# Optimization experiments

Measured on AMD Instinct MI355X. Metric: run time of the kernel, lower is better.

## Reference

```python
import jax, jax.numpy as jnp
import numpy as np

B, D, T, H = 1024, 128, 256, 64  # batch, input_dim, seq_len, hidden_dim


def _lstm_layer(x_proj, w_hh):
    """x_proj: [B, T, 4H] precomputed input projection (incl. both biases).
    Returns (all hidden states [B, T, H], final hidden [B, H])."""
    b = x_proj.shape[0]
    h0 = jnp.zeros((b, H), x_proj.dtype)
    c0 = jnp.zeros((b, H), x_proj.dtype)

    def step(carry, xt):
        h, c = carry
        gates = xt + h @ w_hh.T  # [B, 4H]; PyTorch gate order i, f, g, o
        i, f, g, o = jnp.split(gates, 4, axis=-1)
        i = jax.nn.sigmoid(i)
        f = jax.nn.sigmoid(f)
        g = jnp.tanh(g)
        o = jax.nn.sigmoid(o)
        c = f * c + i * g
        h = o * jnp.tanh(c)
        return (h, c), h

    (hT, _), ys = jax.lax.scan(step, (h0, c0), x_proj.transpose(1, 0, 2))
    return ys.transpose(1, 0, 2), hT


def setup_inputs() -> dict:
    key = jax.random.key(0)
    ks = jax.random.split(key, 11)
    s = 1.0 / np.sqrt(H)  # PyTorch LSTM init scale
    return {
        "x": jax.random.normal(ks[0], (B, D, T), jnp.float32),
        "w_ih0": jax.random.normal(ks[1], (4 * H, D), jnp.float32) * s,
        "w_hh0": jax.random.normal(ks[2], (4 * H, H), jnp.float32) * s,
        "b_ih0": jax.random.normal(ks[3], (4 * H,), jnp.float32) * s,
        "b_hh0": jax.random.normal(ks[4], (4 * H,), jnp.float32) * s,
        "w_ih1": jax.random.normal(ks[5], (4 * H, H), jnp.float32) * s,
        "w_hh1": jax.random.normal(ks[6], (4 * H, H), jnp.float32) * s,
        "b_ih1": jax.random.normal(ks[7], (4 * H,), jnp.float32) * s,
        "b_hh1": jax.random.normal(ks[8], (4 * H,), jnp.float32) * s,
        "w_fc": jax.random.normal(ks[9], (D, H), jnp.float32) * s,
        "b_fc": jax.random.normal(ks[10], (D,), jnp.float32) * s,
    }


def reference(x, w_ih0, w_hh0, b_ih0, b_hh0, w_ih1, w_hh1, b_ih1, b_hh1, w_fc, b_fc):
    # x: [B, input_dim, T] -> permute(0, 2, 1) -> [B, T, input_dim]
    xt = x.transpose(0, 2, 1)
    # Layer 0: precompute input projection for all timesteps (one big GEMM)
    xp0 = xt @ w_ih0.T + (b_ih0 + b_hh0)  # [B, T, 4H]
    ys0, _ = _lstm_layer(xp0, w_hh0)
    # Inter-layer dropout(p=0.3) is identity in eval/inference mode.
    xp1 = ys0 @ w_ih1.T + (b_ih1 + b_hh1)  # [B, T, 4H]
    _, hT = _lstm_layer(xp1, w_hh1)
    # Final-timestep linear head: lstm_out[:, -1, :] == final hidden state hT
    scores = hT @ w_fc.T + b_fc  # [B, input_dim]
    return scores
```

## Files before the change

### kernel.cpp

```cpp
#include <hip/hip_runtime.h>

#define T_SEQ 256
#define PH  72
#define HSZ 1152

typedef __bf16 bf16x8 __attribute__((ext_vector_type(8)));
typedef float f32x4 __attribute__((ext_vector_type(4)));
typedef _Float16 f16x8 __attribute__((ext_vector_type(8)));

__device__ __forceinline__ float b2f(unsigned short u) {
    union { unsigned int i; float f; } v; v.i = ((unsigned int)u) << 16; return v.f;
}
__device__ __forceinline__ unsigned short f2b(float f) {
    unsigned int x = __builtin_bit_cast(unsigned int, f);
    unsigned int r = (x + 0x7fffu + ((x >> 16) & 1u)) >> 16;
    return (unsigned short)r;
}
__device__ __forceinline__ float sigmoid_f(float x) {
    float e = __builtin_amdgcn_exp2f(-1.4426950408889634f * x);
    return __builtin_amdgcn_rcpf(1.0f + e);
}
__device__ __forceinline__ float tanh_f(float x) {
    float e = __builtin_amdgcn_exp2f(-2.8853900817779268f * x);
    return 2.0f * __builtin_amdgcn_rcpf(1.0f + e) - 1.0f;
}
__device__ __forceinline__ void load_frag16(const float* wp, int n, int K, int k0,
                                            f16x8& hi, f16x8& lo) {
    const float* wf = wp + (size_t)n * K + k0;
    #pragma unroll
    for (int j = 0; j < 8; ++j) {
        const float v = wf[j];
        const _Float16 h = (_Float16)v;
        hi[j] = h;
        lo[j] = (_Float16)(v - (float)h);
    }
}
__device__ __forceinline__ f16x8 load_frag16h(const float* wp, int n, int K, int k0) {
    const float* wf = wp + (size_t)n * K + k0;
    f16x8 h;
    #pragma unroll
    for (int j = 0; j < 8; ++j) h[j] = (_Float16)wf[j];
    return h;
}
__device__ __forceinline__ void load_frag32(const float* wp, int n, int K, int k0,
                                            bf16x8& hi, bf16x8& lo) {
    const float* wf = wp + (size_t)n * K + k0;
    #pragma unroll
    for (int j = 0; j < 8; ++j) {
        const float v = wf[j];
        const unsigned short h = f2b(v);
        hi[j] = __builtin_bit_cast(__bf16, h);
        lo[j] = __builtin_bit_cast(__bf16, f2b(v - b2f(h)));
    }
}
__device__ __forceinline__ void gload16(const void* g, void* l) {
    __builtin_amdgcn_global_load_lds(
        (const __attribute__((address_space(1))) unsigned int*)g,
        (__attribute__((address_space(3))) unsigned int*)l, 16, 0, 0);
}

#define MFMA(a, b, c)   __builtin_amdgcn_mfma_f32_16x16x32_bf16(a, b, c, 0, 0, 0)
#define MFMA16(a, b, c) __builtin_amdgcn_mfma_f32_16x16x32_f16(a, b, c, 0, 0, 0)

#define XTD 136
#define XRW 4376
__global__ __launch_bounds__(512, 2) void proj0_kernel(
    const float* __restrict__ x, const float* __restrict__ wih0,
    const float* __restrict__ bih0, const float* __restrict__ bhh0,
    _Float16* __restrict__ xp)
{
    __shared__ _Float16 xh[16 * XRW];
    const int bb  = blockIdx.x >> 3;
    const int tch = (blockIdx.x & 7) * 32;
    const int tid = threadIdx.x, lane = tid & 63, wv = tid >> 6;
    const int l16 = lane & 15, quad = lane >> 4, k0 = quad * 8;
    const int wl = wv >> 1, gp = wv & 1;

    f16x8 fwh[2][4];
    float gb[2];
    #pragma unroll
    for (int gg = 0; gg < 2; ++gg) {
        const int n = (gp * 2 + gg) * 64 + wl * 16 + l16;
        #pragma unroll
        for (int ks = 0; ks < 4; ++ks)
            fwh[gg][ks] = load_frag16h(wih0, n, 128, ks * 32 + k0);
        gb[gg] = bih0[n] + bhh0[n];
    }

    #pragma unroll 4
    for (int it = 0; it < 32; ++it) {
        const int e = it * 512 + tid;
        const int tq = e & 7, d = (e >> 3) & 127, row = e >> 10;
        const float4 v = *(const float4*)(x +
            ((size_t)(bb * 16 + row) * 128 + d) * 256 + tch + tq * 4);
        const float vv[4] = {v.x, v.y, v.z, v.w};
        #pragma unroll
        for (int j = 0; j < 4; ++j)
            xh[row * XRW + (tq * 4 + j) * XTD + d] = (_Float16)vv[j];
    }
    __syncthreads();

    for (int t = 0; t < 32; ++t) {
        f16x8 a_h[4];
        #pragma unroll
        for (int ks = 0; ks < 4; ++ks)
            a_h[ks] = *(const f16x8*)&xh[l16 * XRW + t * XTD + ks * 32 + k0];
        f32x4 acc[2];
        #pragma unroll
        for (int gg = 0; gg < 2; ++gg)
            acc[gg] = (f32x4){gb[gg], gb[gg], gb[gg], gb[gg]};
        #pragma unroll
        for (int gg = 0; gg < 2; ++gg)
            #pragma unroll
            for (int ks = 0; ks < 4; ++ks)
                acc[gg] = MFMA16(a_h[ks], fwh[gg][ks], acc[gg]);
        f16x8 o0;
        #pragma unroll
        for (int gg = 0; gg < 2; ++gg)
            #pragma unroll
            for (int r = 0; r < 4; ++r)
                o0[gg * 4 + r] = (_Float16)acc[gg][r];
        *(f16x8*)(xp + (size_t)(bb * 256 + tch + t) * 4096 + gp * 2048
                  + (wl * 64 + quad * 16 + l16) * 8) = o0;
    }
}

__global__ __launch_bounds__(512, 2) void rec_kernel(
    const _Float16* __restrict__ xp,
    const float* __restrict__ whh0, const float* __restrict__ wih1,
    const float* __restrict__ whh1, const float* __restrict__ bih1,
    const float* __restrict__ bhh1, const float* __restrict__ wfc,
    const float* __restrict__ bfc, float* __restrict__ out)
{
    __shared__ _Float16 xpl[8 * 4096];
    __shared__ _Float16 h0[2 * HSZ], h1[2 * HSZ];
    const int tid = threadIdx.x, lane = tid & 63, w = tid >> 6;
    const int l16 = lane & 15, quad = lane >> 4, k0 = quad * 8;
    const int wl = w & 3;
    const bool is1 = (w < 4);
    const int bb  = blockIdx.x & 63;
    const int sub = blockIdx.x >> 6;

    const char* gxp = (const char*)(xp + (size_t)bb * 256 * 4096);
    char* xplB = (char*)xpl;

    if (!is1) {
        #pragma unroll
        for (int t = 0; t < 8; ++t)
            #pragma unroll
            for (int c2 = 0; c2 < 2; ++c2)
                gload16(gxp + (size_t)t * 8192 + (wl * 2 + c2) * 1024 + lane * 16,
                        xplB + t * 8192 + (wl * 2 + c2) * 1024);
    }

    f16x8 fAh[4][2], fAl[4][2], fBh[4][2], fBl[4][2];
    float gb1[4] = {0.f, 0.f, 0.f, 0.f};
    #pragma unroll
    for (int g = 0; g < 4; ++g) {
        const int n = g * 64 + wl * 16 + l16;
        if (is1) {
            #pragma unroll
            for (int ks = 0; ks < 2; ++ks) {
                fAh[g][ks] = load_frag16h(wih1, n, 64, ks * 32 + k0);
                load_frag16(whh1, n, 64, ks * 32 + k0, fBh[g][ks], fBl[g][ks]);
            }
            gb1[g] = bih1[n] + bhh1[n];
        } else {
            #pragma unroll
            for (int ks = 0; ks < 2; ++ks)
                load_frag16(whh0, n, 64, ks * 32 + k0, fAh[g][ks], fAl[g][ks]);
        }
    }
    for (int i = tid; i < 2 * HSZ; i += 512) { h0[i] = (_Float16)0.f; h1[i] = (_Float16)0.f; }
    float c = 0.f;
    const int gbh = (wl * 64 + quad * 16 + l16) * 8;

    __syncthreads();

    if (!is1) {
        const float xi = (float)xpl[gbh + sub];
        const float xg = (float)xpl[2048 + gbh + sub];
        const float xo = (float)xpl[2048 + gbh + 4 + sub];
        const float gi = sigmoid_f(xi);
        const float gg = tanh_f(xg);
        const float go = sigmoid_f(xo);
        c = gi * gg;
        h0[(quad * 4) * PH + wl * 16 + l16] = (_Float16)(go * tanh_f(c));
    }
    __syncthreads();

    for (int t = 0; t < 255; ++t) {
        const int s0 = t & 1, s1 = s0 ^ 1;
        const int tn = t + 1;
        if (is1) {
            f16x8 ah[2], bh[2];
            #pragma unroll
            for (int ks = 0; ks < 2; ++ks) {
                ah[ks] = *(const f16x8*)&h0[s0 * HSZ + l16 * PH + ks * 32 + k0];
                bh[ks] = *(const f16x8*)&h1[s1 * HSZ + l16 * PH + ks * 32 + k0];
            }
            f32x4 acc[4];
            #pragma unroll
            for (int g = 0; g < 4; ++g)
                acc[g] = (f32x4){gb1[g], 0.f, 0.f, 0.f};
            #pragma unroll
            for (int g = 0; g < 4; ++g)
                #pragma unroll
                for (int ks = 0; ks < 2; ++ks) {
                    acc[g] = MFMA16(ah[ks], fAh[g][ks], acc[g]);
                    acc[g] = MFMA16(bh[ks], fBh[g][ks], acc[g]);
                    acc[g] = MFMA16(bh[ks], fBl[g][ks], acc[g]);
                }
            const float gi = sigmoid_f(acc[0][0]);
            const float gf = sigmoid_f(acc[1][0]);
            const float gg = tanh_f(acc[2][0]);
            const float go = sigmoid_f(acc[3][0]);
            c = gf * c + gi * gg;
            h1[s0 * HSZ + (quad * 4) * PH + wl * 16 + l16] =
                (_Float16)(go * tanh_f(c));
        } else {
            if ((tn & 3) == 0) {
                const int cc = (tn >> 2) + 1;
                if (cc < 64) {
                    #pragma unroll
                    for (int t2 = 0; t2 < 4; ++t2)
                        #pragma unroll
                        for (int c2 = 0; c2 < 2; ++c2)
                            gload16(gxp + (size_t)(cc * 4 + t2) * 8192
                                        + (wl * 2 + c2) * 1024 + lane * 16,
                                    xplB + ((cc & 1) * 4 + t2) * 8192
                                        + (wl * 2 + c2) * 1024);
                }
            }
            const int sb = (((tn >> 2) & 1) * 4 + (tn & 3)) * 4096 + gbh;
            const float xi = (float)xpl[sb + sub];
            const float xf = (float)xpl[sb + 4 + sub];
            const float xg = (float)xpl[sb + 2048 + sub];
            const float xo = (float)xpl[sb + 2048 + 4 + sub];
            f16x8 ah[2];
            #pragma unroll
            for (int ks = 0; ks < 2; ++ks)
                ah[ks] = *(const f16x8*)&h0[s0 * HSZ + l16 * PH + ks * 32 + k0];
            f32x4 acc[4];
            acc[0] = (f32x4){xi, 0.f, 0.f, 0.f};
            acc[1] = (f32x4){xf, 0.f, 0.f, 0.f};
            acc[2] = (f32x4){xg, 0.f, 0.f, 0.f};
            acc[3] = (f32x4){xo, 0.f, 0.f, 0.f};
            #pragma unroll
            for (int g = 0; g < 4; ++g)
                #pragma unroll
                for (int ks = 0; ks < 2; ++ks) {
                    acc[g] = MFMA16(ah[ks], fAh[g][ks], acc[g]);
                    acc[g] = MFMA16(ah[ks], fAl[g][ks], acc[g]);
                }
            const float gi = sigmoid_f(acc[0][0]);
            const float gf = sigmoid_f(acc[1][0]);
            const float gg = tanh_f(acc[2][0]);
            const float go = sigmoid_f(acc[3][0]);
            c = gf * c + gi * gg;
            h0[s1 * HSZ + (quad * 4) * PH + wl * 16 + l16] =
                (_Float16)(go * tanh_f(c));
        }
        __syncthreads();
    }

    if (is1) {
        f16x8 ah[2], bh[2];
        #pragma unroll
        for (int ks = 0; ks < 2; ++ks) {
            ah[ks] = *(const f16x8*)&h0[HSZ + l16 * PH + ks * 32 + k0];
            bh[ks] = *(const f16x8*)&h1[l16 * PH + ks * 32 + k0];
        }
        f32x4 acc[4];
        #pragma unroll
        for (int g = 0; g < 4; ++g)
            acc[g] = (f32x4){gb1[g], 0.f, 0.f, 0.f};
        #pragma unroll
        for (int g = 0; g < 4; ++g)
            #pragma unroll
            for (int ks = 0; ks < 2; ++ks) {
                acc[g] = MFMA16(ah[ks], fAh[g][ks], acc[g]);
                acc[g] = MFMA16(bh[ks], fBh[g][ks], acc[g]);
                acc[g] = MFMA16(bh[ks], fBl[g][ks], acc[g]);
            }
        const float gi = sigmoid_f(acc[0][0]);
        const float gf = sigmoid_f(acc[1][0]);
        const float gg = tanh_f(acc[2][0]);
        const float go = sigmoid_f(acc[3][0]);
        c = gf * c + gi * gg;
        h1[HSZ + (quad * 4) * PH + wl * 16 + l16] = (_Float16)(go * tanh_f(c));
    }
    __syncthreads();

    const int n   = tid & 127;
    const int sel = tid >> 7;
    float s = 0.f;
    for (int k = 0; k < 64; ++k)
        s += (float)h1[HSZ + (sel * 4) * PH + k] * wfc[n * 64 + k];
    out[(size_t)(bb * 16 + sel * 4 + sub) * 128 + n] = s + bfc[n];
}

#define XPT 136
#define XPI 4360
__global__ __launch_bounds__(256, 1) void mega_fb(
    const float* __restrict__ x,
    const float* wih0p, const float* whh0p, const float* bih0p, const float* bhh0p,
    const float* wih1p, const float* whh1p, const float* bih1p, const float* bhh1p,
    const float* wfcp, const float* bfcp, float* out)
{
    extern __shared__ __align__(16) unsigned short smem[];
    unsigned short* xs  = smem;
    unsigned short* h0h = smem + 16 * XPI;
    unsigned short* h0o = h0h + 2 * HSZ;
    unsigned short* h1h = h0h + 4 * HSZ;
    unsigned short* h1o = h0h + 6 * HSZ;

    const int tid = threadIdx.x, lane = tid & 63, w = tid >> 6;
    const int l16 = lane & 15, quad = lane >> 4;
    const int b0 = blockIdx.x * 16, k0 = quad * 8;

    bf16x8 fih0h[4][4], fih0l[4][4], fhh0h[4][2], fhh0l[4][2];
    bf16x8 fih1h[4][2], fih1l[4][2], fhh1h[4][2], fhh1l[4][2];
    float gb0r[4], gb1r[4];
    #pragma unroll
    for (int g = 0; g < 4; ++g) {
        const int n = g * 64 + w * 16 + l16;
        #pragma unroll
        for (int ks = 0; ks < 4; ++ks)
            load_frag32(wih0p, n, 128, ks * 32 + k0, fih0h[g][ks], fih0l[g][ks]);
        #pragma unroll
        for (int ks = 0; ks < 2; ++ks) {
            load_frag32(whh0p, n, 64, ks * 32 + k0, fhh0h[g][ks], fhh0l[g][ks]);
            load_frag32(wih1p, n, 64, ks * 32 + k0, fih1h[g][ks], fih1l[g][ks]);
            load_frag32(whh1p, n, 64, ks * 32 + k0, fhh1h[g][ks], fhh1l[g][ks]);
        }
        gb0r[g] = bih0p[n] + bhh0p[n];
        gb1r[g] = bih1p[n] + bhh1p[n];
    }
    for (int i = tid; i < 8 * HSZ; i += 256) h0h[i] = 0;
    float c0[4] = {0.f, 0.f, 0.f, 0.f}, c1[4] = {0.f, 0.f, 0.f, 0.f};

    for (int tc = 0; tc < 16; ++tc) {
        __syncthreads();
        for (int l = 0; l < 32; ++l) {
            const int e = l * 256 + tid;
            const int cc = e & 3, d = (e >> 2) & 127, i = e >> 9;
            const float4 v = *(const float4*)(x +
                (((size_t)(b0 + i) * 128 + d) * 256 + tc * 16 + cc * 4));
            const float vv[4] = {v.x, v.y, v.z, v.w};
            #pragma unroll
            for (int j = 0; j < 4; ++j) {
                const unsigned short hi = f2b(vv[j]);
                xs[i * XPI + (cc * 4 + j) * XPT + d] = hi;
                xs[i * XPI + 2176 + (cc * 4 + j) * XPT + d] = f2b(vv[j] - b2f(hi));
            }
        }
        __syncthreads();
        for (int tt = 0; tt < 16; ++tt) {
            const int t = tc * 16 + tt;
            const int p = t & 1, q = p ^ 1;
            bf16x8 xa[4], xo[4], hh[2], ho[2];
            #pragma unroll
            for (int ks = 0; ks < 4; ++ks) {
                xa[ks] = *(const bf16x8*)&xs[l16 * XPI + tt * XPT + ks * 32 + k0];
                xo[ks] = *(const bf16x8*)&xs[l16 * XPI + 2176 + tt * XPT + ks * 32 + k0];
            }
            #pragma unroll
            for (int ks = 0; ks < 2; ++ks) {
                hh[ks] = *(const bf16x8*)&h0h[p * HSZ + l16 * PH + ks * 32 + k0];
                ho[ks] = *(const bf16x8*)&h0o[p * HSZ + l16 * PH + ks * 32 + k0];
            }
            f32x4 acc[4];
            #pragma unroll
            for (int g = 0; g < 4; ++g)
                acc[g] = (f32x4){gb0r[g], gb0r[g], gb0r[g], gb0r[g]};
            #pragma unroll
            for (int g = 0; g < 4; ++g) {
                #pragma unroll
                for (int ks = 0; ks < 4; ++ks) {
                    acc[g] = MFMA(xa[ks], fih0h[g][ks], acc[g]);
                    acc[g] = MFMA(xa[ks], fih0l[g][ks], acc[g]);
                    acc[g] = MFMA(xo[ks], fih0h[g][ks], acc[g]);
                }
                #pragma unroll
                for (int ks = 0; ks < 2; ++ks) {
                    acc[g] = MFMA(hh[ks], fhh0h[g][ks], acc[g]);
                    acc[g] = MFMA(ho[ks], fhh0h[g][ks], acc[g]);
                    acc[g] = MFMA(hh[ks], fhh0l[g][ks], acc[g]);
                }
            }
            #pragma unroll
            for (int r = 0; r < 4; ++r) {
                const float gi = sigmoid_f(acc[0][r]);
                const float gf = sigmoid_f(acc[1][r]);
                const float gg = tanh_f(acc[2][r]);
                const float go = sigmoid_f(acc[3][r]);
                c0[r] = gf * c0[r] + gi * gg;
                const float hv = go * tanh_f(c0[r]);
                const unsigned short hb = f2b(hv);
                const int idx = q * HSZ + (quad * 4 + r) * PH + w * 16 + l16;
                h0h[idx] = hb; h0o[idx] = f2b(hv - b2f(hb));
            }
            __syncthreads();
            bf16x8 ah[2], ao[2], bh[2], bo[2];
            #pragma unroll
            for (int ks = 0; ks < 2; ++ks) {
                ah[ks] = *(const bf16x8*)&h0h[q * HSZ + l16 * PH + ks * 32 + k0];
                ao[ks] = *(const bf16x8*)&h0o[q * HSZ + l16 * PH + ks * 32 + k0];
                bh[ks] = *(const bf16x8*)&h1h[p * HSZ + l16 * PH + ks * 32 + k0];
                bo[ks] = *(const bf16x8*)&h1o[p * HSZ + l16 * PH + ks * 32 + k0];
            }
            #pragma unroll
            for (int g = 0; g < 4; ++g)
                acc[g] = (f32x4){gb1r[g], gb1r[g], gb1r[g], gb1r[g]};
            #pragma unroll
            for (int g = 0; g < 4; ++g)
                #pragma unroll
                for (int ks = 0; ks < 2; ++ks) {
                    acc[g] = MFMA(ah[ks], fih1h[g][ks], acc[g]);
                    acc[g] = MFMA(ao[ks], fih1h[g][ks], acc[g]);
                    acc[g] = MFMA(bh[ks], fhh1h[g][ks], acc[g]);
                    acc[g] = MFMA(bo[ks], fhh1h[g][ks], acc[g]);
                    acc[g] = MFMA(ah[ks], fih1l[g][ks], acc[g]);
                    acc[g] = MFMA(bh[ks], fhh1l[g][ks], acc[g]);
                }
            #pragma unroll
            for (int r = 0; r < 4; ++r) {
                const float gi = sigmoid_f(acc[0][r]);
                const float gf = sigmoid_f(acc[1][r]);
                const float gg = tanh_f(acc[2][r]);
                const float go = sigmoid_f(acc[3][r]);
                c1[r] = gf * c1[r] + gi * gg;
                const float hv = go * tanh_f(c1[r]);
                const unsigned short hb = f2b(hv);
                const int idx = q * HSZ + (quad * 4 + r) * PH + w * 16 + l16;
                h1h[idx] = hb; h1o[idx] = f2b(hv - b2f(hb));
            }
            __syncthreads();
        }
    }
    const int n = tid & 127;
    const int mb = (tid >> 7) * 8;
    float s[8] = {0.f, 0.f, 0.f, 0.f, 0.f, 0.f, 0.f, 0.f};
    for (int k = 0; k < 64; ++k) {
        const float wv = wfcp[n * 64 + k];
        #pragma unroll
        for (int m = 0; m < 8; ++m) {
            const int idx = (mb + m) * PH + k;
            s[m] += (b2f(h1h[idx]) + b2f(h1o[idx])) * wv;
        }
    }
    #pragma unroll
    for (int m = 0; m < 8; ++m)
        out[(size_t)(b0 + mb + m) * 128 + n] = s[m] + bfcp[n];
}

extern "C" void kernel_launch(void* const* d_in, const int* in_sizes, int n_in,
                              void* d_out, int out_size, void* d_ws, size_t ws_size,
                              hipStream_t stream) {
    const float* x     = (const float*)d_in[0];
    const float* wih0  = (const float*)d_in[1];
    const float* whh0  = (const float*)d_in[2];
    const float* bih0  = (const float*)d_in[3];
    const float* bhh0  = (const float*)d_in[4];
    const float* wih1  = (const float*)d_in[5];
    const float* whh1  = (const float*)d_in[6];
    const float* bih1  = (const float*)d_in[7];
    const float* bhh1  = (const float*)d_in[8];
    const float* wfc   = (const float*)d_in[9];
    const float* bfc   = (const float*)d_in[10];
    float* out = (float*)d_out;

    const size_t xp_bytes = (size_t)1024 * 256 * 256 * sizeof(_Float16);
    if (ws_size >= xp_bytes) {
        _Float16* xp = (_Float16*)d_ws;
        proj0_kernel<<<512, 512, 0, stream>>>(x, wih0, bih0, bhh0, xp);
        rec_kernel<<<256, 512, 0, stream>>>(xp, whh0, wih1, whh1, bih1, bhh1,
                                            wfc, bfc, out);
    } else {
        const size_t lds_bytes = (16 * XPI + 8 * HSZ) * sizeof(unsigned short);
        mega_fb<<<64, 256, lds_bytes, stream>>>(x, wih0, whh0, bih0, bhh0,
                                                wih1, whh1, bih1, bhh1, wfc, bfc, out);
    }
}
```

Measured before the change: 427.8 us.

## Fuse layer-0 input projection into recurrent kernel and drop workspace fallback

Removes the separate proj0 kernel that wrote a 128 MB fp16 gate-projection buffer to workspace. The recurrent kernel now stages raw x into LDS in 16-step chunks, double-buffered with register prefetch. Layer-0 waves compute x·W_ih0 with MFMA each step alongside the hidden-state product. This removes the global write and read of the projection buffer and one launch. In exchange, layer-0 waves do extra MFMAs and LDS traffic on the serial critical path and hold more weight registers. The bf16 mega fallback kernel is also deleted.

New measurement: 567.3 us. 32.6% more time.

```diff
diff --git a/kernel.cpp b/kernel.cpp
--- a/kernel.cpp
+++ b/kernel.cpp
@@ -3,19 +3,12 @@
 #define T_SEQ 256
 #define PH  72
 #define HSZ 1152
-
-typedef __bf16 bf16x8 __attribute__((ext_vector_type(8)));
+#define XRW 144
+#define XSL (4 * XRW)
+
 typedef float f32x4 __attribute__((ext_vector_type(4)));
 typedef _Float16 f16x8 __attribute__((ext_vector_type(8)));
 
-__device__ __forceinline__ float b2f(unsigned short u) {
-    union { unsigned int i; float f; } v; v.i = ((unsigned int)u) << 16; return v.f;
-}
-__device__ __forceinline__ unsigned short f2b(float f) {
-    unsigned int x = __builtin_bit_cast(unsigned int, f);
-    unsigned int r = (x + 0x7fffu + ((x >> 16) & 1u)) >> 16;
-    return (unsigned short)r;
-}
 __device__ __forceinline__ float sigmoid_f(float x) {
     float e = __builtin_amdgcn_exp2f(-1.4426950408889634f * x);
     return __builtin_amdgcn_rcpf(1.0f + e);
@@ -23,6 +16,13 @@
 __device__ __forceinline__ float tanh_f(float x) {
     float e = __builtin_amdgcn_exp2f(-2.8853900817779268f * x);
     return 2.0f * __builtin_amdgcn_rcpf(1.0f + e) - 1.0f;
+}
+__device__ __forceinline__ f16x8 load_frag16h(const float* wp, int n, int K, int k0) {
+    const float* wf = wp + (size_t)n * K + k0;
+    f16x8 h;
+    #pragma unroll
+    for (int j = 0; j < 8; ++j) h[j] = (_Float16)wf[j];
+    return h;
 }
 __device__ __forceinline__ void load_frag16(const float* wp, int n, int K, int k0,
                                             f16x8& hi, f16x8& lo) {
@@ -35,104 +35,19 @@
         lo[j] = (_Float16)(v - (float)h);
     }
 }
-__device__ __forceinline__ f16x8 load_frag16h(const float* wp, int n, int K, int k0) {
-    const float* wf = wp + (size_t)n * K + k0;
-    f16x8 h;
-    #pragma unroll
-    for (int j = 0; j < 8; ++j) h[j] = (_Float16)wf[j];
-    return h;
-}
-__device__ __forceinline__ void load_frag32(const float* wp, int n, int K, int k0,
-                                            bf16x8& hi, bf16x8& lo) {
-    const float* wf = wp + (size_t)n * K + k0;
-    #pragma unroll
-    for (int j = 0; j < 8; ++j) {
-        const float v = wf[j];
-        const unsigned short h = f2b(v);
-        hi[j] = __builtin_bit_cast(__bf16, h);
-        lo[j] = __builtin_bit_cast(__bf16, f2b(v - b2f(h)));
-    }
-}
-__device__ __forceinline__ void gload16(const void* g, void* l) {
-    __builtin_amdgcn_global_load_lds(
-        (const __attribute__((address_space(1))) unsigned int*)g,
-        (__attribute__((address_space(3))) unsigned int*)l, 16, 0, 0);
-}
-
-#define MFMA(a, b, c)   __builtin_amdgcn_mfma_f32_16x16x32_bf16(a, b, c, 0, 0, 0)
+
 #define MFMA16(a, b, c) __builtin_amdgcn_mfma_f32_16x16x32_f16(a, b, c, 0, 0, 0)
 
-#define XTD 136
-#define XRW 4376
-__global__ __launch_bounds__(512, 2) void proj0_kernel(
-    const float* __restrict__ x, const float* __restrict__ wih0,
+__global__ __launch_bounds__(512, 2) void rec_fused(
+    const float* __restrict__ x,
+    const float* __restrict__ wih0, const float* __restrict__ whh0,
     const float* __restrict__ bih0, const float* __restrict__ bhh0,
-    _Float16* __restrict__ xp)
+    const float* __restrict__ wih1, const float* __restrict__ whh1,
+    const float* __restrict__ bih1, const float* __restrict__ bhh1,
+    const float* __restrict__ wfc,  const float* __restrict__ bfc,
+    float* __restrict__ out)
 {
-    __shared__ _Float16 xh[16 * XRW];
-    const int bb  = blockIdx.x >> 3;
-    const int tch = (blockIdx.x & 7) * 32;
-    const int tid = threadIdx.x, lane = tid & 63, wv = tid >> 6;
-    const int l16 = lane & 15, quad = lane >> 4, k0 = quad * 8;
-    const int wl = wv >> 1, gp = wv & 1;
-
-    f16x8 fwh[2][4];
-    float gb[2];
-    #pragma unroll
-    for (int gg = 0; gg < 2; ++gg) {
-        const int n = (gp * 2 + gg) * 64 + wl * 16 + l16;
-        #pragma unroll
-        for (int ks = 0; ks < 4; ++ks)
-            fwh[gg][ks] = load_frag16h(wih0, n, 128, ks * 32 + k0);
-        gb[gg] = bih0[n] + bhh0[n];
-    }
-
-    #pragma unroll 4
-    for (int it = 0; it < 32; ++it) {
-        const int e = it * 512 + tid;
-        const int tq = e & 7, d = (e >> 3) & 127, row = e >> 10;
-        const float4 v = *(const float4*)(x +
-            ((size_t)(bb * 16 + row) * 128 + d) * 256 + tch + tq * 4);
-        const float vv[4] = {v.x, v.y, v.z, v.w};
-        #pragma unroll
-        for (int j = 0; j < 4; ++j)
-            xh[row * XRW + (tq * 4 + j) * XTD + d] = (_Float16)vv[j];
-    }
-    __syncthreads();
-
-    for (int t = 0; t < 32; ++t) {
-        f16x8 a_h[4];
-        #pragma unroll
-        for (int ks = 0; ks < 4; ++ks)
-            a_h[ks] = *(const f16x8*)&xh[l16 * XRW + t * XTD + ks * 32 + k0];
-        f32x4 acc[2];
-        #pragma unroll
-        for (int gg = 0; gg < 2; ++gg)
-            acc[gg] = (f32x4){gb[gg], gb[gg], gb[gg], gb[gg]};
-        #pragma unroll
-        for (int gg = 0; gg < 2; ++gg)
-            #pragma unroll
-            for (int ks = 0; ks < 4; ++ks)
-                acc[gg] = MFMA16(a_h[ks], fwh[gg][ks], acc[gg]);
-        f16x8 o0;
-        #pragma unroll
-        for (int gg = 0; gg < 2; ++gg)
-            #pragma unroll
-            for (int r = 0; r < 4; ++r)
-                o0[gg * 4 + r] = (_Float16)acc[gg][r];
-        *(f16x8*)(xp + (size_t)(bb * 256 + tch + t) * 4096 + gp * 2048
-                  + (wl * 64 + quad * 16 + l16) * 8) = o0;
-    }
-}
-
-__global__ __launch_bounds__(512, 2) void rec_kernel(
-    const _Float16* __restrict__ xp,
-    const float* __restrict__ whh0, const float* __restrict__ wih1,
-    const float* __restrict__ whh1, const float* __restrict__ bih1,
-    const float* __restrict__ bhh1, const float* __restrict__ wfc,
-    const float* __restrict__ bfc, float* __restrict__ out)
-{
-    __shared__ _Float16 xpl[8 * 4096];
+    __shared__ _Float16 xh[32 * XSL];
     __shared__ _Float16 h0[2 * HSZ], h1[2 * HSZ];
     const int tid = threadIdx.x, lane = tid & 63, w = tid >> 6;
     const int l16 = lane & 15, quad = lane >> 4, k0 = quad * 8;
@@ -141,20 +56,10 @@
     const int bb  = blockIdx.x & 63;
     const int sub = blockIdx.x >> 6;
 
-    const char* gxp = (const char*)(xp + (size_t)bb * 256 * 4096);
-    char* xplB = (char*)xpl;
-
-    if (!is1) {
-        #pragma unroll
-        for (int t = 0; t < 8; ++t)
-            #pragma unroll
-            for (int c2 = 0; c2 < 2; ++c2)
-                gload16(gxp + (size_t)t * 8192 + (wl * 2 + c2) * 1024 + lane * 16,
-                        xplB + t * 8192 + (wl * 2 + c2) * 1024);
-    }
-
-    f16x8 fAh[4][2], fAl[4][2], fBh[4][2], fBl[4][2];
-    float gb1[4] = {0.f, 0.f, 0.f, 0.f};
+    const float* xrow = x + (size_t)(bb * 16 + wl * 4 + sub) * 128 * 256;
+
+    f16x8 fX[4][4], fAh[4][2], fAl[4][2], fBh[4][2], fBl[4][2];
+    float gb[4];
     #pragma unroll
     for (int g = 0; g < 4; ++g) {
         const int n = g * 64 + wl * 16 + l16;
@@ -164,26 +69,57 @@
                 fAh[g][ks] = load_frag16h(wih1, n, 64, ks * 32 + k0);
                 load_frag16(whh1, n, 64, ks * 32 + k0, fBh[g][ks], fBl[g][ks]);
             }
-            gb1[g] = bih1[n] + bhh1[n];
+            gb[g] = bih1[n] + bhh1[n];
         } else {
+            #pragma unroll
+            for (int ks = 0; ks < 4; ++ks)
+                fX[g][ks] = load_frag16h(wih0, n, 128, ks * 32 + k0);
             #pragma unroll
             for (int ks = 0; ks < 2; ++ks)
                 load_frag16(whh0, n, 64, ks * 32 + k0, fAh[g][ks], fAl[g][ks]);
+            gb[g] = bih0[n] + bhh0[n];
         }
     }
     for (int i = tid; i < 2 * HSZ; i += 512) { h0[i] = (_Float16)0.f; h1[i] = (_Float16)0.f; }
     float c = 0.f;
-    const int gbh = (wl * 64 + quad * 16 + l16) * 8;
-
+
+    if (!is1) {
+        #pragma unroll
+        for (int cc = 0; cc < 2; ++cc)
+            #pragma unroll
+            for (int hd = 0; hd < 2; ++hd) {
+                const int d = lane + hd * 64;
+                const float* p = xrow + (size_t)d * 256 + cc * 16;
+                float f[16];
+                #pragma unroll
+                for (int q = 0; q < 4; ++q) {
+                    const float4 v = ((const float4*)p)[q];
+                    f[q * 4 + 0] = v.x; f[q * 4 + 1] = v.y;
+                    f[q * 4 + 2] = v.z; f[q * 4 + 3] = v.w;
+                }
+                #pragma unroll
+                for (int tt = 0; tt < 16; ++tt)
+                    xh[(cc * 16 + tt) * XSL + wl * XRW + d] = (_Float16)f[tt];
+            }
+    }
     __syncthreads();
 
     if (!is1) {
-        const float xi = (float)xpl[gbh + sub];
-        const float xg = (float)xpl[2048 + gbh + sub];
-        const float xo = (float)xpl[2048 + gbh + 4 + sub];
-        const float gi = sigmoid_f(xi);
-        const float gg = tanh_f(xg);
-        const float go = sigmoid_f(xo);
+        f16x8 ax[4];
+        #pragma unroll
+        for (int ks = 0; ks < 4; ++ks)
+            ax[ks] = *(const f16x8*)&xh[(l16 >> 2) * XRW + ks * 32 + k0];
+        f32x4 acc[4];
+        #pragma unroll
+        for (int g = 0; g < 4; ++g) acc[g] = (f32x4){gb[g], 0.f, 0.f, 0.f};
+        #pragma unroll
+        for (int g = 0; g < 4; ++g)
+            #pragma unroll
+            for (int ks = 0; ks < 4; ++ks)
+                acc[g] = MFMA16(ax[ks], fX[g][ks], acc[g]);
+        const float gi = sigmoid_f(acc[0][0]);
+        const float gg = tanh_f(acc[2][0]);
+        const float go = sigmoid_f(acc[3][0]);
         c = gi * gg;
         h0[(quad * 4) * PH + wl * 16 + l16] = (_Float16)(go * tanh_f(c));
     }
@@ -202,7 +138,7 @@
             f32x4 acc[4];
             #pragma unroll
             for (int g = 0; g < 4; ++g)
-                acc[g] = (f32x4){gb1[g], 0.f, 0.f, 0.f};
+                acc[g] = (f32x4){gb[g], 0.f, 0.f, 0.f};
             #pragma unroll
             for (int g = 0; g < 4; ++g)
                 #pragma unroll
@@ -219,40 +155,40 @@
             h1[s0 * HSZ + (quad * 4) * PH + wl * 16 + l16] =
                 (_Float16)(go * tanh_f(c));
         } else {
-            if ((tn & 3) == 0) {
-                const int cc = (tn >> 2) + 1;
-                if (cc < 64) {
+            const bool do_stage = ((tn & 15) == 0) && (tn < 240);
+            float4 vst[8];
+            if (do_stage) {
+                const int cc = (tn >> 4) + 1;
+                #pragma unroll
+                for (int hd = 0; hd < 2; ++hd) {
+                    const float* p = xrow + (size_t)(lane + hd * 64) * 256 + cc * 16;
                     #pragma unroll
-                    for (int t2 = 0; t2 < 4; ++t2)
-                        #pragma unroll
-                        for (int c2 = 0; c2 < 2; ++c2)
-                            gload16(gxp + (size_t)(cc * 4 + t2) * 8192
-                                        + (wl * 2 + c2) * 1024 + lane * 16,
-                                    xplB + ((cc & 1) * 4 + t2) * 8192
-                                        + (wl * 2 + c2) * 1024);
-                }
-            }
-            const int sb = (((tn >> 2) & 1) * 4 + (tn & 3)) * 4096 + gbh;
-            const float xi = (float)xpl[sb + sub];
-            const float xf = (float)xpl[sb + 4 + sub];
-            const float xg = (float)xpl[sb + 2048 + sub];
-            const float xo = (float)xpl[sb + 2048 + 4 + sub];
-            f16x8 ah[2];
+                    for (int q = 0; q < 4; ++q)
+                        vst[hd * 4 + q] = ((const float4*)p)[q];
+                }
+            }
+            const int slot = ((tn >> 4) & 1) * 16 + (tn & 15);
+            f16x8 ax[4], ah[2];
+            #pragma unroll
+            for (int ks = 0; ks < 4; ++ks)
+                ax[ks] = *(const f16x8*)&xh[slot * XSL + (l16 >> 2) * XRW + ks * 32 + k0];
             #pragma unroll
             for (int ks = 0; ks < 2; ++ks)
                 ah[ks] = *(const f16x8*)&h0[s0 * HSZ + l16 * PH + ks * 32 + k0];
             f32x4 acc[4];
-            acc[0] = (f32x4){xi, 0.f, 0.f, 0.f};
-            acc[1] = (f32x4){xf, 0.f, 0.f, 0.f};
-            acc[2] = (f32x4){xg, 0.f, 0.f, 0.f};
-            acc[3] = (f32x4){xo, 0.f, 0.f, 0.f};
-            #pragma unroll
-            for (int g = 0; g < 4; ++g)
+            #pragma unroll
+            for (int g = 0; g < 4; ++g) acc[g] = (f32x4){gb[g], 0.f, 0.f, 0.f};
+            #pragma unroll
+            for (int g = 0; g < 4; ++g) {
+                #pragma unroll
+                for (int ks = 0; ks < 4; ++ks)
+                    acc[g] = MFMA16(ax[ks], fX[g][ks], acc[g]);
                 #pragma unroll
                 for (int ks = 0; ks < 2; ++ks) {
                     acc[g] = MFMA16(ah[ks], fAh[g][ks], acc[g]);
                     acc[g] = MFMA16(ah[ks], fAl[g][ks], acc[g]);
                 }
+            }
             const float gi = sigmoid_f(acc[0][0]);
             const float gf = sigmoid_f(acc[1][0]);
             const float gg = tanh_f(acc[2][0]);
@@ -260,6 +196,22 @@
             c = gf * c + gi * gg;
             h0[s1 * HSZ + (quad * 4) * PH + wl * 16 + l16] =
                 (_Float16)(go * tanh_f(c));
+            if (do_stage) {
+                const int cc = (tn >> 4) + 1;
+                const int sb = (cc & 1) * 16;
+                #pragma unroll
+                for (int hd = 0; hd < 2; ++hd) {
+                    const int d = lane + hd * 64;
+                    #pragma unroll
+                    for (int q = 0; q < 4; ++q) {
+                        const float4 v = vst[hd * 4 + q];
+                        const float vv[4] = {v.x, v.y, v.z, v.w};
+                        #pragma unroll
+                        for (int j = 0; j < 4; ++j)
+                            xh[(sb + q * 4 + j) * XSL + wl * XRW + d] = (_Float16)vv[j];
+                    }
+                }
+            }
         }
         __syncthreads();
     }
@@ -274,7 +226,7 @@
         f32x4 acc[4];
         #pragma unroll
         for (int g = 0; g < 4; ++g)
-            acc[g] = (f32x4){gb1[g], 0.f, 0.f, 0.f};
+            acc[g] = (f32x4){gb[g], 0.f, 0.f, 0.f};
         #pragma unroll
         for (int g = 0; g < 4; ++g)
             #pragma unroll
@@ -298,161 +250,6 @@
     for (int k = 0; k < 64; ++k)
         s += (float)h1[HSZ + (sel * 4) * PH + k] * wfc[n * 64 + k];
     out[(size_t)(bb * 16 + sel * 4 + sub) * 128 + n] = s + bfc[n];
-}
-
-#define XPT 136
-#define XPI 4360
-__global__ __launch_bounds__(256, 1) void mega_fb(
-    const float* __restrict__ x,
-    const float* wih0p, const float* whh0p, const float* bih0p, const float* bhh0p,
-    const float* wih1p, const float* whh1p, const float* bih1p, const float* bhh1p,
-    const float* wfcp, const float* bfcp, float* out)
-{
-    extern __shared__ __align__(16) unsigned short smem[];
-    unsigned short* xs  = smem;
-    unsigned short* h0h = smem + 16 * XPI;
-    unsigned short* h0o = h0h + 2 * HSZ;
-    unsigned short* h1h = h0h + 4 * HSZ;
-    unsigned short* h1o = h0h + 6 * HSZ;
-
-    const int tid = threadIdx.x, lane = tid & 63, w = tid >> 6;
-    const int l16 = lane & 15, quad = lane >> 4;
-    const int b0 = blockIdx.x * 16, k0 = quad * 8;
-
-    bf16x8 fih0h[4][4], fih0l[4][4], fhh0h[4][2], fhh0l[4][2];
-    bf16x8 fih1h[4][2], fih1l[4][2], fhh1h[4][2], fhh1l[4][2];
-    float gb0r[4], gb1r[4];
-    #pragma unroll
-    for (int g = 0; g < 4; ++g) {
-        const int n = g * 64 + w * 16 + l16;
-        #pragma unroll
-        for (int ks = 0; ks < 4; ++ks)
-            load_frag32(wih0p, n, 128, ks * 32 + k0, fih0h[g][ks], fih0l[g][ks]);
-        #pragma unroll
-        for (int ks = 0; ks < 2; ++ks) {
-            load_frag32(whh0p, n, 64, ks * 32 + k0, fhh0h[g][ks], fhh0l[g][ks]);
-            load_frag32(wih1p, n, 64, ks * 32 + k0, fih1h[g][ks], fih1l[g][ks]);
-            load_frag32(whh1p, n, 64, ks * 32 + k0, fhh1h[g][ks], fhh1l[g][ks]);
-        }
-        gb0r[g] = bih0p[n] + bhh0p[n];
-        gb1r[g] = bih1p[n] + bhh1p[n];
-    }
-    for (int i = tid; i < 8 * HSZ; i += 256) h0h[i] = 0;
-    float c0[4] = {0.f, 0.f, 0.f, 0.f}, c1[4] = {0.f, 0.f, 0.f, 0.f};
-
-    for (int tc = 0; tc < 16; ++tc) {
-        __syncthreads();
-        for (int l = 0; l < 32; ++l) {
-            const int e = l * 256 + tid;
-            const int cc = e & 3, d = (e >> 2) & 127, i = e >> 9;
-            const float4 v = *(const float4*)(x +
-                (((size_t)(b0 + i) * 128 + d) * 256 + tc * 16 + cc * 4));
-            const float vv[4] = {v.x, v.y, v.z, v.w};
-            #pragma unroll
-            for (int j = 0; j < 4; ++j) {
-                const unsigned short hi = f2b(vv[j]);
-                xs[i * XPI + (cc * 4 + j) * XPT + d] = hi;
-                xs[i * XPI + 2176 + (cc * 4 + j) * XPT + d] = f2b(vv[j] - b2f(hi));
-            }
-        }
-        __syncthreads();
-        for (int tt = 0; tt < 16; ++tt) {
-            const int t = tc * 16 + tt;
-            const int p = t & 1, q = p ^ 1;
-            bf16x8 xa[4], xo[4], hh[2], ho[2];
-            #pragma unroll
-            for (int ks = 0; ks < 4; ++ks) {
-                xa[ks] = *(const bf16x8*)&xs[l16 * XPI + tt * XPT + ks * 32 + k0];
-                xo[ks] = *(const bf16x8*)&xs[l16 * XPI + 2176 + tt * XPT + ks * 32 + k0];
-            }
-            #pragma unroll
-            for (int ks = 0; ks < 2; ++ks) {
-                hh[ks] = *(const bf16x8*)&h0h[p * HSZ + l16 * PH + ks * 32 + k0];
-                ho[ks] = *(const bf16x8*)&h0o[p * HSZ + l16 * PH + ks * 32 + k0];
-            }
-            f32x4 acc[4];
-            #pragma unroll
-            for (int g = 0; g < 4; ++g)
-                acc[g] = (f32x4){gb0r[g], gb0r[g], gb0r[g], gb0r[g]};
-            #pragma unroll
-            for (int g = 0; g < 4; ++g) {
-                #pragma unroll
-                for (int ks = 0; ks < 4; ++ks) {
-                    acc[g] = MFMA(xa[ks], fih0h[g][ks], acc[g]);
-                    acc[g] = MFMA(xa[ks], fih0l[g][ks], acc[g]);
-                    acc[g] = MFMA(xo[ks], fih0h[g][ks], acc[g]);
-                }
-                #pragma unroll
-                for (int ks = 0; ks < 2; ++ks) {
-                    acc[g] = MFMA(hh[ks], fhh0h[g][ks], acc[g]);
-                    acc[g] = MFMA(ho[ks], fhh0h[g][ks], acc[g]);
-                    acc[g] = MFMA(hh[ks], fhh0l[g][ks], acc[g]);
-                }
-            }
-            #pragma unroll
-            for (int r = 0; r < 4; ++r) {
-                const float gi = sigmoid_f(acc[0][r]);
-                const float gf = sigmoid_f(acc[1][r]);
-                const float gg = tanh_f(acc[2][r]);
-                const float go = sigmoid_f(acc[3][r]);
-                c0[r] = gf * c0[r] + gi * gg;
-                const float hv = go * tanh_f(c0[r]);
-                const unsigned short hb = f2b(hv);
-                const int idx = q * HSZ + (quad * 4 + r) * PH + w * 16 + l16;
-                h0h[idx] = hb; h0o[idx] = f2b(hv - b2f(hb));
-            }
-            __syncthreads();
-            bf16x8 ah[2], ao[2], bh[2], bo[2];
-            #pragma unroll
-            for (int ks = 0; ks < 2; ++ks) {
-                ah[ks] = *(const bf16x8*)&h0h[q * HSZ + l16 * PH + ks * 32 + k0];
-                ao[ks] = *(const bf16x8*)&h0o[q * HSZ + l16 * PH + ks * 32 + k0];
-                bh[ks] = *(const bf16x8*)&h1h[p * HSZ + l16 * PH + ks * 32 + k0];
-                bo[ks] = *(const bf16x8*)&h1o[p * HSZ + l16 * PH + ks * 32 + k0];
-            }
-            #pragma unroll
-            for (int g = 0; g < 4; ++g)
-                acc[g] = (f32x4){gb1r[g], gb1r[g], gb1r[g], gb1r[g]};
-            #pragma unroll
-            for (int g = 0; g < 4; ++g)
-                #pragma unroll
-                for (int ks = 0; ks < 2; ++ks) {
-                    acc[g] = MFMA(ah[ks], fih1h[g][ks], acc[g]);
-                    acc[g] = MFMA(ao[ks], fih1h[g][ks], acc[g]);
-                    acc[g] = MFMA(bh[ks], fhh1h[g][ks], acc[g]);
-                    acc[g] = MFMA(bo[ks], fhh1h[g][ks], acc[g]);
-                    acc[g] = MFMA(ah[ks], fih1l[g][ks], acc[g]);
-                    acc[g] = MFMA(bh[ks], fhh1l[g][ks], acc[g]);
-                }
-            #pragma unroll
-            for (int r = 0; r < 4; ++r) {
-                const float gi = sigmoid_f(acc[0][r]);
-                const float gf = sigmoid_f(acc[1][r]);
-                const float gg = tanh_f(acc[2][r]);
-                const float go = sigmoid_f(acc[3][r]);
-                c1[r] = gf * c1[r] + gi * gg;
-                const float hv = go * tanh_f(c1[r]);
-                const unsigned short hb = f2b(hv);
-                const int idx = q * HSZ + (quad * 4 + r) * PH + w * 16 + l16;
-                h1h[idx] = hb; h1o[idx] = f2b(hv - b2f(hb));
-            }
-            __syncthreads();
-        }
-    }
-    const int n = tid & 127;
-    const int mb = (tid >> 7) * 8;
-    float s[8] = {0.f, 0.f, 0.f, 0.f, 0.f, 0.f, 0.f, 0.f};
-    for (int k = 0; k < 64; ++k) {
-        const float wv = wfcp[n * 64 + k];
-        #pragma unroll
-        for (int m = 0; m < 8; ++m) {
-            const int idx = (mb + m) * PH + k;
-            s[m] += (b2f(h1h[idx]) + b2f(h1o[idx])) * wv;
-        }
-    }
-    #pragma unroll
-    for (int m = 0; m < 8; ++m)
-        out[(size_t)(b0 + mb + m) * 128 + n] = s[m] + bfcp[n];
 }
 
 extern "C" void kernel_launch(void* const* d_in, const int* in_sizes, int n_in,
@@ -471,15 +268,6 @@
     const float* bfc   = (const float*)d_in[10];
     float* out = (float*)d_out;
 
-    const size_t xp_bytes = (size_t)1024 * 256 * 256 * sizeof(_Float16);
-    if (ws_size >= xp_bytes) {
-        _Float16* xp = (_Float16*)d_ws;
-        proj0_kernel<<<512, 512, 0, stream>>>(x, wih0, bih0, bhh0, xp);
-        rec_kernel<<<256, 512, 0, stream>>>(xp, whh0, wih1, whh1, bih1, bhh1,
-                                            wfc, bfc, out);
-    } else {
-        const size_t lds_bytes = (16 * XPI + 8 * HSZ) * sizeof(unsigned short);
-        mega_fb<<<64, 256, lds_bytes, stream>>>(x, wih0, whh0, bih0, bhh0,
-                                                wih1, whh1, bih1, bhh1, wfc, bfc, out);
-    }
-}
+    rec_fused<<<256, 512, 0, stream>>>(x, wih0, whh0, bih0, bhh0,
+                                       wih1, whh1, bih1, bhh1, wfc, bfc, out);
+}
```
